# Performance work log

Hardware: AMD Instinct MI355X
Metric: run time of the kernel (lower is better)

Reference implementation:

```python
import jax, jax.numpy as jnp
import numpy as np

B, C, T = 8, 8, 2048
WIN = 512
F_BINS = WIN // 2 + 1  # 257
H, NH = 256, 4
DH = H // NH
EPS = 1e-4


def _ln(x, g, b):
    m = jnp.mean(x, -1, keepdims=True)
    v = jnp.var(x, -1, keepdims=True)
    return (x - m) / jnp.sqrt(v + 1e-5) * g + b


def setup_inputs() -> dict:
    key = jax.random.key(0)
    ks = jax.random.split(key, 16)
    w = lambda i, shape: jax.random.normal(ks[i], shape, jnp.float32) * 0.02
    return {
        'x': jax.random.normal(ks[0], (B, C, T, F_BINS), jnp.float32),
        'W_in': w(1, (F_BINS, H)), 'b_in': jnp.zeros((H,), jnp.float32),
        'W_out': w(2, (H, F_BINS)), 'b_out': jnp.zeros((F_BINS,), jnp.float32),
        'Wq': w(3, (H, H)), 'bq': jnp.zeros((H,), jnp.float32),
        'Wk': w(4, (H, H)), 'bk': jnp.zeros((H,), jnp.float32),
        'Wv': w(5, (H, H)), 'bv': jnp.zeros((H,), jnp.float32),
        'Wo': w(6, (H, H)), 'bo': jnp.zeros((H,), jnp.float32),
        'ln1_g': jnp.ones((H,), jnp.float32), 'ln1_b': jnp.zeros((H,), jnp.float32),
        'Wf1': w(7, (H, WIN)), 'bf1': jnp.zeros((WIN,), jnp.float32),
        'Wf2': w(8, (WIN, H)), 'bf2': jnp.zeros((H,), jnp.float32),
        'ln2_g': jnp.ones((H,), jnp.float32), 'ln2_b': jnp.zeros((H,), jnp.float32),
        'Ws1': w(9, (H, H // 2)), 'bs1': jnp.zeros((H // 2,), jnp.float32),
        'Ws2': w(10, (H // 2, 1)), 'bs2': jnp.zeros((1,), jnp.float32),
        'ps_a': jnp.zeros((1,), jnp.float32), 'ps_b': jnp.ones((1,), jnp.float32),
    }


def _forward(x, W_in, b_in, W_out, b_out, Wq, bq, Wk, bk, Wv, bv, Wo, bo,
             ln1_g, ln1_b, Wf1, bf1, Wf2, bf2, ln2_g, ln2_b,
             Ws1, bs1, Ws2, bs2, ps_a, ps_b):
    lin1 = jax.nn.relu(x @ W_in + b_in)  # [B,C,T,H]
    b, c, t, h_dim = lin1.shape

    def encoder(q, kv):
        # q: [B,T,H], kv: [B,Cc,T,H]; per-time-frame attention over channels
        cc = kv.shape[1]
        Q = (q @ Wq + bq).reshape(b, t, NH, DH)
        K = (kv @ Wk + bk).reshape(b, cc, t, NH, DH)
        V = (kv @ Wv + bv).reshape(b, cc, t, NH, DH)
        scores = jnp.einsum('bthd,bcthd->bthc', Q, K) / jnp.sqrt(jnp.float32(DH))
        A = jax.nn.softmax(scores, axis=-1)
        ctx = jnp.einsum('bthc,bcthd->bthd', A, V).reshape(b, t, h_dim)
        h1 = _ln(q + ctx @ Wo + bo, ln1_g, ln1_b)
        f = jax.nn.relu(h1 @ Wf1 + bf1) @ Wf2 + bf2
        return _ln(h1 + f, ln2_g, ln2_b)

    def seen_enough(hh):
        s = jax.nn.relu(hh @ Ws1 + bs1) @ Ws2 + bs2
        return jax.nn.sigmoid((s - ps_a) / (ps_b + 1e-8))

    still = jnp.ones((b, t, 1), jnp.float32)
    cum = jnp.zeros((b, t, 1), jnp.float32)
    rem = jnp.ones((b, t, 1), jnp.float32)
    pc = jnp.zeros((b, t, 1), jnp.float32)
    out = jnp.zeros((b, t, h_dim), jnp.float32)
    gate = jnp.float32(1.0)  # replicates data-dependent early break

    for ci in range(c):  # small fixed loop over mic channels (ACT ponder)
        hh = encoder(lin1[:, ci], lin1[:, :ci + 1])
        cur = seen_enough(hh) if ci < c - 1 else jnp.ones((b, t, 1), jnp.float32)
        cum_n = cum + cur * still
        pc_n = pc + still
        still_n = (cum_n < 1 - EPS).astype(jnp.float32)
        out_n = out + hh * (cur * still_n + rem * (1 - still_n))
        rem_n = rem - cur * still_n
        pc_n = pc_n + rem_n * (1 - still_n)
        live = gate > 0.5
        cum = jnp.where(live, cum_n, cum)
        pc = jnp.where(live, pc_n, pc)
        out = jnp.where(live, out_n, out)
        rem = jnp.where(live, rem_n, rem)
        still = jnp.where(live, still_n, still)
        gate = gate * (jnp.sum(still) >= EPS).astype(jnp.float32)

    encoder_out = jax.nn.relu(out @ W_out + b_out)  # [B,T,F]
    return encoder_out, pc[:, :, 0]


def reference(x, W_in, b_in, W_out, b_out, Wq, bq, Wk, bk, Wv, bv, Wo, bo,
              ln1_g, ln1_b, Wf1, bf1, Wf2, bf2, ln2_g, ln2_b,
              Ws1, bs1, Ws2, bs2, ps_a, ps_b):
    return _forward(x, W_in, b_in, W_out, b_out, Wq, bq, Wk, bk, Wv, bv, Wo, bo,
                    ln1_g, ln1_b, Wf1, bf1, Wf2, bf2, ln2_g, ln2_b,
                    Ws1, bs1, Ws2, bs2, ps_a, ps_b)
```

## Files before the change

kernel.cpp:

```cpp
#include <hip/hip_runtime.h>
#include <hip/hip_bf16.h>
#include <math.h>

typedef _Float16 f16;
typedef _Float16 f16x4 __attribute__((ext_vector_type(4)));
typedef _Float16 f16x8 __attribute__((ext_vector_type(8)));
typedef float f32x16 __attribute__((ext_vector_type(16)));

constexpr int CH = 8;
constexpr int TT = 2048;
constexpr int FB = 257;
constexpr int HD = 256;
constexpr int DHD = 64;
constexpr int WN = 512;
constexpr int HF = 128;
constexpr int RR = 8 * TT;
constexpr int KXP = 288;

template<int ACT, int WF32, int WF16, int QKV, int XSRC>
__global__ __launch_bounds__(256, 2) void gemm2(
    const f16* __restrict__ Ahi, const f16* __restrict__ Alo, int K,
    const float* __restrict__ Axf, long agrp,
    const f16* __restrict__ Bp,
    const float* __restrict__ bias, const float* __restrict__ bias1,
    const float* __restrict__ bias2,
    float* __restrict__ C0, float* __restrict__ C1, float* __restrict__ C2,
    int ldc, f16* __restrict__ Chi, f16* __restrict__ Clo, int ldf,
    int Nreal, const int* __restrict__ alive)
{
  if (alive && *alive == 0) return;
  __shared__ f16 As[2][2][128][40];
  const int tid = threadIdx.x;
  const int m0 = blockIdx.x * 128;
  const int n0 = blockIdx.y * 64;
  const int q = tid & 3, r = tid >> 2;
  const int lane = tid & 63, wm = tid >> 6;
  const int lr = lane & 31, lg = lane >> 5;
  const int nb0 = n0 >> 5, kd8 = K >> 3;

  f32x16 acc[2];
  #pragma unroll
  for (int nf = 0; nf < 2; nf++)
    #pragma unroll
    for (int g = 0; g < 16; g++) acc[nf][g] = 0.f;

  const long aoff = (long)(m0 + r) * K + q * 8;
  const long hstep = (long)64 * K;
  const float* xR0 = nullptr;
  const float* xR1 = nullptr;
  if constexpr (XSRC) {
    const int r0 = m0 + r, r1 = r0 + 64;
    xR0 = Axf + (long)(r0 >> 11) * agrp + (long)(r0 & 2047) * FB;
    xR1 = Axf + (long)(r1 >> 11) * agrp + (long)(r1 & 2047) * FB;
  }

  f16x8 sA[4];
  auto loadA = [&](int k0) {
    if constexpr (XSRC) {
      float a0[8], a1[8];
      #pragma unroll
      for (int j = 0; j < 8; j++) {
        const int k = k0 + q * 8 + j;
        a0[j] = (k < FB) ? xR0[k] : 0.f;
        a1[j] = (k < FB) ? xR1[k] : 0.f;
      }
      #pragma unroll
      for (int j = 0; j < 8; j++) {
        const f16 h0 = (f16)a0[j]; sA[0][j] = h0; sA[2][j] = (f16)(a0[j] - (float)h0);
        const f16 h1 = (f16)a1[j]; sA[1][j] = h1; sA[3][j] = (f16)(a1[j] - (float)h1);
      }
    } else {
      const long a = aoff + k0;
      sA[0] = *(const f16x8*)(Ahi + a);  sA[1] = *(const f16x8*)(Ahi + a + hstep);
      sA[2] = *(const f16x8*)(Alo + a);  sA[3] = *(const f16x8*)(Alo + a + hstep);
    }
  };
  auto loadB = [&](f16x8 B[2][2][2], int k0) {
    const int kb = (k0 >> 3) + lg;
    #pragma unroll
    for (int kh = 0; kh < 2; kh++)
      #pragma unroll
      for (int nf = 0; nf < 2; nf++)
        #pragma unroll
        for (int hl = 0; hl < 2; hl++)
          B[kh][nf][hl] = *(const f16x8*)(Bp +
              ((long)((nb0 + nf) * kd8 + kb + kh * 2) * 512 + hl * 256 + lr * 8));
  };
  auto kstep = [&](f16x8 SB[2][2][2], f16x8 TB[2][2][2], int k0, int d) {
    *(f16x8*)&As[d][0][r][q * 8]      = sA[0];
    *(f16x8*)&As[d][0][r + 64][q * 8] = sA[1];
    *(f16x8*)&As[d][1][r][q * 8]      = sA[2];
    *(f16x8*)&As[d][1][r + 64][q * 8] = sA[3];
    __syncthreads();
    if (k0 + 32 < K) { loadA(k0 + 32); loadB(TB, k0 + 32); }
    f16x8 fa[2][2];
    #pragma unroll
    for (int kh = 0; kh < 2; kh++)
      #pragma unroll
      for (int hl = 0; hl < 2; hl++)
        fa[kh][hl] = *(const f16x8*)&As[d][hl][wm * 32 + lr][kh * 16 + lg * 8];
    #pragma unroll
    for (int kh = 0; kh < 2; kh++)
      #pragma unroll
      for (int nf = 0; nf < 2; nf++) {
        acc[nf] = __builtin_amdgcn_mfma_f32_32x32x16_f16(fa[kh][1], SB[kh][nf][0], acc[nf], 0, 0, 0);
        acc[nf] = __builtin_amdgcn_mfma_f32_32x32x16_f16(fa[kh][0], SB[kh][nf][1], acc[nf], 0, 0, 0);
        acc[nf] = __builtin_amdgcn_mfma_f32_32x32x16_f16(fa[kh][0], SB[kh][nf][0], acc[nf], 0, 0, 0);
      }
  };

  f16x8 B0[2][2][2], B1[2][2][2];
  loadA(0);
  loadB(B0, 0);
  int d = 0;
  for (int k0 = 0; k0 < K; k0 += 64) {
    kstep(B0, B1, k0, d); d ^= 1;
    if (k0 + 32 < K) { kstep(B1, B0, k0 + 32, d); d ^= 1; }
  }

  #pragma unroll
  for (int nf = 0; nf < 2; nf++) {
    const int col = n0 + nf * 32 + lr;
    const float* bp = bias;
    float* Cp = C0;
    int cc = col;
    if (QKV) {
      const int sel = col >> 8;
      cc = col & 255;
      Cp = sel == 0 ? C0 : (sel == 1 ? C1 : C2);
      bp = sel == 0 ? bias : (sel == 1 ? bias1 : bias2);
    }
    const float bb = (col < Nreal) ? bp[cc] : 0.f;
    #pragma unroll
    for (int g = 0; g < 16; g++) {
      const long row = m0 + wm * 32 + (g & 3) + 8 * (g >> 2) + 4 * lg;
      float v = acc[nf][g] + bb;
      if (ACT) v = fmaxf(v, 0.f);
      if (col < Nreal) {
        if (WF32) Cp[row * (long)ldc + cc] = v;
        if (WF16) {
          const f16 hi = (f16)v;
          Chi[row * (long)ldf + col] = hi;
          Clo[row * (long)ldf + col] = (f16)(v - (float)hi);
        }
      }
    }
  }
}

__global__ __launch_bounds__(512) void gemm_ln(
    const f16* __restrict__ Ahi, const f16* __restrict__ Alo, int K,
    const f16* __restrict__ Bp, const float* __restrict__ bias,
    const f16* __restrict__ Rhi, const f16* __restrict__ Rlo,
    const float* __restrict__ gg, const float* __restrict__ bb_,
    f16* __restrict__ Ohi, f16* __restrict__ Olo,
    const int* __restrict__ alive)
{
  if (alive && *alive == 0) return;
  __shared__ f16 As[2][2][64][40];
  __shared__ float red[64][4][2];
  const int tid = threadIdx.x;
  const int m0 = blockIdx.x * 64;
  const int lane = tid & 63, wave = tid >> 6;
  const int wm = wave & 1, wn = wave >> 1;
  const int lr = lane & 31, lg = lane >> 5;
  const int srow = tid >> 3, sk = (tid & 7) * 4;
  const int kd8 = K >> 3;

  f32x16 acc[2];
  #pragma unroll
  for (int nf = 0; nf < 2; nf++)
    #pragma unroll
    for (int g = 0; g < 16; g++) acc[nf][g] = 0.f;

  const f16* arh = Ahi + (long)(m0 + srow) * K + sk;
  const f16* arl = Alo + (long)(m0 + srow) * K + sk;
  f16x4 sAh, sAl;
  auto loadA = [&](int k0) {
    sAh = *(const f16x4*)(arh + k0);
    sAl = *(const f16x4*)(arl + k0);
  };
  auto loadB = [&](f16x8 B[2][2][2], int k0) {
    const int kb = (k0 >> 3) + lg;
    #pragma unroll
    for (int kh = 0; kh < 2; kh++)
      #pragma unroll
      for (int nf = 0; nf < 2; nf++)
        #pragma unroll
        for (int hl = 0; hl < 2; hl++)
          B[kh][nf][hl] = *(const f16x8*)(Bp +
              ((long)((wn * 2 + nf) * kd8 + kb + kh * 2) * 512 + hl * 256 + lr * 8));
  };
  auto kstep = [&](f16x8 SB[2][2][2], f16x8 TB[2][2][2], int k0, int d) {
    *(f16x4*)&As[d][0][srow][sk] = sAh;
    *(f16x4*)&As[d][1][srow][sk] = sAl;
    __syncthreads();
    if (k0 + 32 < K) { loadA(k0 + 32); loadB(TB, k0 + 32); }
    f16x8 fa[2][2];
    #pragma unroll
    for (int kh = 0; kh < 2; kh++)
      #pragma unroll
      for (int hl = 0; hl < 2; hl++)
        fa[kh][hl] = *(const f16x8*)&As[d][hl][wm * 32 + lr][kh * 16 + lg * 8];
    #pragma unroll
    for (int kh = 0; kh < 2; kh++)
      #pragma unroll
      for (int nf = 0; nf < 2; nf++) {
        acc[nf] = __builtin_amdgcn_mfma_f32_32x32x16_f16(fa[kh][1], SB[kh][nf][0], acc[nf], 0, 0, 0);
        acc[nf] = __builtin_amdgcn_mfma_f32_32x32x16_f16(fa[kh][0], SB[kh][nf][1], acc[nf], 0, 0, 0);
        acc[nf] = __builtin_amdgcn_mfma_f32_32x32x16_f16(fa[kh][0], SB[kh][nf][0], acc[nf], 0, 0, 0);
      }
  };

  f16x8 B0[2][2][2], B1[2][2][2];
  loadA(0);
  loadB(B0, 0);
  int d = 0;
  for (int k0 = 0; k0 < K; k0 += 64) {
    kstep(B0, B1, k0, d); d ^= 1;
    if (k0 + 32 < K) { kstep(B1, B0, k0 + 32, d); d ^= 1; }
  }

  float pr[16], qr[16];
  #pragma unroll
  for (int g = 0; g < 16; g++) {
    const int row_l = wm * 32 + (g & 3) + 8 * (g >> 2) + 4 * lg;
    const long rbase = (long)(m0 + row_l) * HD;
    float s = 0.f, sq = 0.f;
    #pragma unroll
    for (int nf = 0; nf < 2; nf++) {
      const int col = wn * 64 + nf * 32 + lr;
      float v = acc[nf][g] + bias[col]
              + (float)Rhi[rbase + col] + (float)Rlo[rbase + col];
      acc[nf][g] = v;
      s += v; sq += v * v;
    }
    pr[g] = s; qr[g] = sq;
  }
  #pragma unroll
  for (int g = 0; g < 16; g++)
    #pragma unroll
    for (int i = 1; i <= 16; i <<= 1) {
      pr[g] += __shfl_xor(pr[g], i, 64);
      qr[g] += __shfl_xor(qr[g], i, 64);
    }
  if (lr == 0) {
    #pragma unroll
    for (int g = 0; g < 16; g++) {
      const int row_l = wm * 32 + (g & 3) + 8 * (g >> 2) + 4 * lg;
      red[row_l][wn][0] = pr[g];
      red[row_l][wn][1] = qr[g];
    }
  }
  __syncthreads();
  #pragma unroll
  for (int g = 0; g < 16; g++) {
    const int row_l = wm * 32 + (g & 3) + 8 * (g >> 2) + 4 * lg;
    const float mean = (red[row_l][0][0] + red[row_l][1][0] +
                        red[row_l][2][0] + red[row_l][3][0]) * (1.f / HD);
    const float ex2 = (red[row_l][0][1] + red[row_l][1][1] +
                       red[row_l][2][1] + red[row_l][3][1]) * (1.f / HD);
    const float inv = 1.f / sqrtf(ex2 - mean * mean + 1e-5f);
    const long rbase = (long)(m0 + row_l) * HD;
    #pragma unroll
    for (int nf = 0; nf < 2; nf++) {
      const int col = wn * 64 + nf * 32 + lr;
      const float o = (acc[nf][g] - mean) * inv * gg[col] + bb_[col];
      const f16 hi = (f16)o;
      Ohi[rbase + col] = hi;
      Olo[rbase + col] = (f16)(o - (float)hi);
    }
  }
}

template<int FIRST>
__global__ __launch_bounds__(256) void s1_act(
    const f16* __restrict__ hhhi, const f16* __restrict__ hhlo,
    const f16* __restrict__ Bp, const float* __restrict__ bs1,
    const float* __restrict__ Ws2, const float* __restrict__ bs2,
    const float* __restrict__ psa, const float* __restrict__ psb,
    float* __restrict__ cum, float* __restrict__ rem,
    float* __restrict__ still, float* __restrict__ pc,
    f16* __restrict__ outhi, f16* __restrict__ outlo,
    float* __restrict__ pcdst,
    const int* __restrict__ alive, int* __restrict__ myFlag)
{
  if (!FIRST && alive && *alive == 0) return;
  __shared__ f16 As[2][2][64][40];
  __shared__ float red[64][2];
  const int tid = threadIdx.x;
  const int m0 = blockIdx.x * 64;
  const int lane = tid & 63, wave = tid >> 6;
  const int wm = wave & 1, wn = wave >> 1;
  const int lr = lane & 31, lg = lane >> 5;
  const int srow = tid >> 2, sk = (tid & 3) * 8;
  const int K = HD, kd8 = K >> 3;

  f32x16 acc[2];
  #pragma unroll
  for (int nf = 0; nf < 2; nf++)
    #pragma unroll
    for (int g = 0; g < 16; g++) acc[nf][g] = 0.f;

  const f16* arh = hhhi + (long)(m0 + srow) * K + sk;
  const f16* arl = hhlo + (long)(m0 + srow) * K + sk;
  f16x8 sAh, sAl;
  auto loadA = [&](int k0) {
    sAh = *(const f16x8*)(arh + k0);
    sAl = *(const f16x8*)(arl + k0);
  };
  auto loadB = [&](f16x8 B[2][2][2], int k0) {
    const int kb = (k0 >> 3) + lg;
    #pragma unroll
    for (int kh = 0; kh < 2; kh++)
      #pragma unroll
      for (int nf = 0; nf < 2; nf++)
        #pragma unroll
        for (int hl = 0; hl < 2; hl++)
          B[kh][nf][hl] = *(const f16x8*)(Bp +
              ((long)((wn * 2 + nf) * kd8 + kb + kh * 2) * 512 + hl * 256 + lr * 8));
  };
  auto kstep = [&](f16x8 SB[2][2][2], f16x8 TB[2][2][2], int k0, int d) {
    *(f16x8*)&As[d][0][srow][sk] = sAh;
    *(f16x8*)&As[d][1][srow][sk] = sAl;
    __syncthreads();
    if (k0 + 32 < K) { loadA(k0 + 32); loadB(TB, k0 + 32); }
    f16x8 fa[2][2];
    #pragma unroll
    for (int kh = 0; kh < 2; kh++)
      #pragma unroll
      for (int hl = 0; hl < 2; hl++)
        fa[kh][hl] = *(const f16x8*)&As[d][hl][wm * 32 + lr][kh * 16 + lg * 8];
    #pragma unroll
    for (int kh = 0; kh < 2; kh++)
      #pragma unroll
      for (int nf = 0; nf < 2; nf++) {
        acc[nf] = __builtin_amdgcn_mfma_f32_32x32x16_f16(fa[kh][1], SB[kh][nf][0], acc[nf], 0, 0, 0);
        acc[nf] = __builtin_amdgcn_mfma_f32_32x32x16_f16(fa[kh][0], SB[kh][nf][1], acc[nf], 0, 0, 0);
        acc[nf] = __builtin_amdgcn_mfma_f32_32x32x16_f16(fa[kh][0], SB[kh][nf][0], acc[nf], 0, 0, 0);
      }
  };

  f16x8 B0[2][2][2], B1[2][2][2];
  loadA(0);
  loadB(B0, 0);
  int d = 0;
  for (int k0 = 0; k0 < K; k0 += 64) {
    kstep(B0, B1, k0, d); d ^= 1;
    if (k0 + 32 < K) { kstep(B1, B0, k0 + 32, d); d ^= 1; }
  }

  float pr[16];
  #pragma unroll
  for (int g = 0; g < 16; g++) {
    float s = 0.f;
    #pragma unroll
    for (int nf = 0; nf < 2; nf++) {
      const int col = wn * 64 + nf * 32 + lr;
      const float v = fmaxf(acc[nf][g] + bs1[col], 0.f);
      s += v * Ws2[col];
    }
    pr[g] = s;
  }
  #pragma unroll
  for (int g = 0; g < 16; g++)
    #pragma unroll
    for (int i = 1; i <= 16; i <<= 1) pr[g] += __shfl_xor(pr[g], i, 64);
  if (lr == 0) {
    #pragma unroll
    for (int g = 0; g < 16; g++) {
      const int row_l = wm * 32 + (g & 3) + 8 * (g >> 2) + 4 * lg;
      red[row_l][wn] = pr[g];
    }
  }
  __syncthreads();

  const float ipsb = 1.f / (psb[0] + 1e-8f);
  const float pa = psa[0], b2 = bs2[0];
  for (int row_l = 0; row_l < 64; row_l++) {
    const long rg = m0 + row_l;
    const float s = red[row_l][0] + red[row_l][1] + b2;
    const float curv = 1.f / (1.f + expf(-(s - pa) * ipsb));
    const float cu = FIRST ? 0.f : cum[rg];
    const float re = FIRST ? 1.f : rem[rg];
    const float st = FIRST ? 1.f : still[rg];
    const float pp = FIRST ? 0.f : pc[rg];
    const float cum_n = cu + curv * st;
    float pc_n = pp + st;
    const float still_n = (cum_n < 0.9999f) ? 1.f : 0.f;
    const float wgt = curv * still_n + re * (1.f - still_n);
    const long idx = rg * HD + tid;
    const float prev = FIRST ? 0.f : ((float)outhi[idx] + (float)outlo[idx]);
    const float hhv = (float)hhhi[idx] + (float)hhlo[idx];
    const float newv = prev + hhv * wgt;
    const f16 hi = (f16)newv;
    outhi[idx] = hi;
    outlo[idx] = (f16)(newv - (float)hi);
    const float rem_n = re - curv * still_n;
    pc_n += rem_n * (1.f - still_n);
    if (tid == 0) {
      cum[rg] = cum_n; rem[rg] = rem_n; still[rg] = still_n; pc[rg] = pc_n;
      pcdst[rg] = pc_n;
      if (still_n > 0.5f) *myFlag = 1;
    }
  }
}

__global__ __launch_bounds__(256) void act_last(
    const f16* __restrict__ hhhi, const f16* __restrict__ hhlo,
    float* __restrict__ cum, float* __restrict__ rem,
    float* __restrict__ still, float* __restrict__ pc,
    f16* __restrict__ outhi, f16* __restrict__ outlo,
    float* __restrict__ pcdst, const int* __restrict__ alive)
{
  if (alive && *alive == 0) return;
  const int tid = threadIdx.x;
  for (int rr = 0; rr < 8; rr++) {
    const long r = (long)blockIdx.x * 8 + rr;
    const float re = rem[r], st = still[r];
    const float cum_n = cum[r] + st;
    float pc_n = pc[r] + st;
    const float still_n = (cum_n < 0.9999f) ? 1.f : 0.f;
    const float wgt = still_n + re * (1.f - still_n);
    const long idx = r * HD + tid;
    const float newv = (float)outhi[idx] + (float)outlo[idx]
                     + ((float)hhhi[idx] + (float)hhlo[idx]) * wgt;
    const f16 hi = (f16)newv;
    outhi[idx] = hi;
    outlo[idx] = (f16)(newv - (float)hi);
    const float rem_n = re - still_n;
    pc_n += rem_n * (1.f - still_n);
    if (tid == 0) {
      cum[r] = cum_n; rem[r] = rem_n; still[r] = still_n; pc[r] = pc_n;
      pcdst[r] = pc_n;
    }
  }
}

__global__ __launch_bounds__(256) void wsplit_k(
    const float* __restrict__ W_in, const float* __restrict__ Wq,
    const float* __restrict__ Wk, const float* __restrict__ Wv,
    const float* __restrict__ Wo, const float* __restrict__ Wf1,
    const float* __restrict__ Wf2, const float* __restrict__ Ws1,
    const float* __restrict__ Wout,
    f16* __restrict__ WinP, f16* __restrict__ WqkvP, f16* __restrict__ WoP,
    f16* __restrict__ Wf1P, f16* __restrict__ Wf2P, f16* __restrict__ Ws1P,
    f16* __restrict__ WoutP)
{
  const int y = blockIdx.y;
  const long idx = (long)blockIdx.x * 256 + threadIdx.x;
  int Npad, Kpad, Ksrc;
  f16* dst;
  switch (y) {
    case 0: Npad = 256; Kpad = 288; Ksrc = 257; dst = WinP;  break;
    case 1: Npad = 768; Kpad = 256; Ksrc = 256; dst = WqkvP; break;
    case 2: Npad = 256; Kpad = 256; Ksrc = 256; dst = WoP;   break;
    case 3: Npad = 512; Kpad = 256; Ksrc = 256; dst = Wf1P;  break;
    case 4: Npad = 256; Kpad = 512; Ksrc = 512; dst = Wf2P;  break;
    case 5: Npad = 128; Kpad = 256; Ksrc = 256; dst = Ws1P;  break;
    default: Npad = 384; Kpad = 256; Ksrc = 256; dst = WoutP; break;
  }
  if (idx >= (long)Npad * Kpad) return;
  const int n = (int)(idx / Kpad), k = (int)(idx % Kpad);
  float v = 0.f;
  if (k < Ksrc) {
    switch (y) {
      case 0: v = W_in[(long)k * 256 + n]; break;
      case 1: { const int sel = n >> 8;
                const float* s = sel == 0 ? Wq : (sel == 1 ? Wk : Wv);
                v = s[(long)k * 256 + (n & 255)]; } break;
      case 2: v = Wo[(long)k * 256 + n]; break;
      case 3: v = Wf1[(long)k * 512 + n]; break;
      case 4: v = Wf2[(long)k * 256 + n]; break;
      case 5: v = Ws1[(long)k * 128 + n]; break;
      default: v = (n < 257) ? Wout[(long)k * 257 + n] : 0.f; break;
    }
  }
  const long base = ((long)(n >> 5) * (Kpad >> 3) + (k >> 3)) * 512 + (n & 31) * 8 + (k & 7);
  const f16 hi = (f16)v;
  dst[base] = hi;
  dst[base + 256] = (f16)(v - (float)hi);
}

template<int NCc>
__global__ __launch_bounds__(256) void attn_k(
    const float* __restrict__ Q, const float* __restrict__ Ksp,
    const float* __restrict__ Vsp, f16* __restrict__ chi,
    f16* __restrict__ clo, const int* __restrict__ alive)
{
  if (alive && *alive == 0) return;
  const int w = threadIdx.x >> 6;
  const int l = threadIdx.x & 63;
  for (int rr = 0; rr < 4; rr++) {
    const long r = (long)blockIdx.x * 4 + rr;
    const float qv = Q[r * HD + w * DHD + l];
    float sc[NCc];
    #pragma unroll
    for (int c = 0; c < NCc; c++) {
      float p = qv * Ksp[((long)c * RR + r) * HD + w * DHD + l];
      #pragma unroll
      for (int s = 32; s > 0; s >>= 1) p += __shfl_xor(p, s, 64);
      sc[c] = p * 0.125f;
    }
    float m = sc[0];
    #pragma unroll
    for (int c = 1; c < NCc; c++) m = fmaxf(m, sc[c]);
    float a[NCc];
    float den = 0.f;
    #pragma unroll
    for (int c = 0; c < NCc; c++) { a[c] = expf(sc[c] - m); den += a[c]; }
    float cv = 0.f;
    #pragma unroll
    for (int c = 0; c < NCc; c++)
      cv = fmaf(a[c] / den, Vsp[((long)c * RR + r) * HD + w * DHD + l], cv);
    const f16 hi = (f16)cv;
    chi[r * HD + w * DHD + l] = hi;
    clo[r * HD + w * DHD + l] = (f16)(cv - (float)hi);
  }
}

__global__ void init_k(int* flags) {
  if (threadIdx.x < 8) flags[threadIdx.x] = 0;
}

extern "C" void kernel_launch(void* const* d_in, const int* in_sizes, int n_in,
                              void* d_out, int out_size, void* d_ws, size_t ws_size,
                              hipStream_t stream) {
  const float* x    = (const float*)d_in[0];
  const float* W_in = (const float*)d_in[1];
  const float* b_in = (const float*)d_in[2];
  const float* W_out= (const float*)d_in[3];
  const float* b_out= (const float*)d_in[4];
  const float* Wq   = (const float*)d_in[5];
  const float* bq   = (const float*)d_in[6];
  const float* Wk   = (const float*)d_in[7];
  const float* bk   = (const float*)d_in[8];
  const float* Wv   = (const float*)d_in[9];
  const float* bv   = (const float*)d_in[10];
  const float* Wo   = (const float*)d_in[11];
  const float* bo   = (const float*)d_in[12];
  const float* ln1g = (const float*)d_in[13];
  const float* ln1b = (const float*)d_in[14];
  const float* Wf1  = (const float*)d_in[15];
  const float* bf1  = (const float*)d_in[16];
  const float* Wf2  = (const float*)d_in[17];
  const float* bf2  = (const float*)d_in[18];
  const float* ln2g = (const float*)d_in[19];
  const float* ln2b = (const float*)d_in[20];
  const float* Ws1  = (const float*)d_in[21];
  const float* bs1  = (const float*)d_in[22];
  const float* Ws2  = (const float*)d_in[23];
  const float* bs2  = (const float*)d_in[24];
  const float* psa  = (const float*)d_in[25];
  const float* psb  = (const float*)d_in[26];

  float* ws = (float*)d_ws;
  long off = 0;
  auto alloc = [&](long n) { float* p = ws + off; off += n; return p; };
  float* Ks   = alloc((long)CH * RR * HD);
  float* Vs   = alloc((long)CH * RR * HD);
  float* Qb   = alloc((long)RR * HD);
  f16* lin1hi = (f16*)alloc((long)RR * HD / 2);
  f16* lin1lo = (f16*)alloc((long)RR * HD / 2);
  f16* ctxhi  = (f16*)alloc((long)RR * HD / 2);
  f16* ctxlo  = (f16*)alloc((long)RR * HD / 2);
  f16* h1hi   = (f16*)alloc((long)RR * HD / 2);
  f16* h1lo   = (f16*)alloc((long)RR * HD / 2);
  f16* hhhi   = (f16*)alloc((long)RR * HD / 2);
  f16* hhlo   = (f16*)alloc((long)RR * HD / 2);
  f16* t1hi   = (f16*)alloc((long)RR * WN / 2);
  f16* t1lo   = (f16*)alloc((long)RR * WN / 2);
  f16* outhi  = (f16*)alloc((long)RR * HD / 2);
  f16* outlo  = (f16*)alloc((long)RR * HD / 2);
  f16* WinP   = (f16*)alloc(2 * 256 * 288 / 2);
  f16* WqkvP  = (f16*)alloc(2 * 768 * 256 / 2);
  f16* WoP    = (f16*)alloc(2 * 256 * 256 / 2);
  f16* Wf1P   = (f16*)alloc(2 * 512 * 256 / 2);
  f16* Wf2P   = (f16*)alloc(2 * 256 * 512 / 2);
  f16* Ws1P   = (f16*)alloc(2 * 128 * 256 / 2);
  f16* WoutP  = (f16*)alloc(2 * 384 * 256 / 2);
  float* cum  = alloc(RR);
  float* rem  = alloc(RR);
  float* still= alloc(RR);
  float* pc   = alloc(RR);
  int* flags  = (int*)alloc(8);

  init_k<<<1, 256, 0, stream>>>(flags);
  wsplit_k<<<dim3(768, 7), 256, 0, stream>>>(
      W_in, Wq, Wk, Wv, Wo, Wf1, Wf2, Ws1, W_out,
      WinP, WqkvP, WoP, Wf1P, Wf2P, Ws1P, WoutP);

  float* pcdst = (float*)d_out + (long)RR * FB;

  for (int ci = 0; ci < CH; ci++) {
    const int* al = (ci == 0) ? nullptr : (flags + ci - 1);
    gemm2<1, 0, 1, 0, 1><<<dim3(128, 4), 256, 0, stream>>>(
        nullptr, nullptr, KXP, x + (long)ci * TT * FB, (long)CH * TT * FB,
        WinP, b_in, b_in, b_in, nullptr, nullptr, nullptr, HD,
        lin1hi, lin1lo, HD, HD, al);
    gemm2<0, 1, 0, 1, 0><<<dim3(128, 12), 256, 0, stream>>>(
        lin1hi, lin1lo, HD, nullptr, 0, WqkvP, bq, bk, bv,
        Qb, Ks + (long)ci * RR * HD, Vs + (long)ci * RR * HD, HD,
        nullptr, nullptr, HD, 768, al);
    switch (ci) {
      case 0: attn_k<1><<<4096, 256, 0, stream>>>(Qb, Ks, Vs, ctxhi, ctxlo, al); break;
      case 1: attn_k<2><<<4096, 256, 0, stream>>>(Qb, Ks, Vs, ctxhi, ctxlo, al); break;
      case 2: attn_k<3><<<4096, 256, 0, stream>>>(Qb, Ks, Vs, ctxhi, ctxlo, al); break;
      case 3: attn_k<4><<<4096, 256, 0, stream>>>(Qb, Ks, Vs, ctxhi, ctxlo, al); break;
      case 4: attn_k<5><<<4096, 256, 0, stream>>>(Qb, Ks, Vs, ctxhi, ctxlo, al); break;
      case 5: attn_k<6><<<4096, 256, 0, stream>>>(Qb, Ks, Vs, ctxhi, ctxlo, al); break;
      case 6: attn_k<7><<<4096, 256, 0, stream>>>(Qb, Ks, Vs, ctxhi, ctxlo, al); break;
      default: attn_k<8><<<4096, 256, 0, stream>>>(Qb, Ks, Vs, ctxhi, ctxlo, al); break;
    }
    gemm_ln<<<256, 512, 0, stream>>>(
        ctxhi, ctxlo, HD, WoP, bo, lin1hi, lin1lo, ln1g, ln1b,
        h1hi, h1lo, al);
    gemm2<1, 0, 1, 0, 0><<<dim3(128, 8), 256, 0, stream>>>(
        h1hi, h1lo, HD, nullptr, 0, Wf1P, bf1, bf1, bf1,
        nullptr, nullptr, nullptr, WN, t1hi, t1lo, WN, WN, al);
    gemm_ln<<<256, 512, 0, stream>>>(
        t1hi, t1lo, WN, Wf2P, bf2, h1hi, h1lo, ln2g, ln2b,
        hhhi, hhlo, al);
    if (ci == 0)
      s1_act<1><<<256, 256, 0, stream>>>(
          hhhi, hhlo, Ws1P, bs1, Ws2, bs2, psa, psb,
          cum, rem, still, pc, outhi, outlo, pcdst, nullptr, flags + 0);
    else if (ci < CH - 1)
      s1_act<0><<<256, 256, 0, stream>>>(
          hhhi, hhlo, Ws1P, bs1, Ws2, bs2, psa, psb,
          cum, rem, still, pc, outhi, outlo, pcdst, al, flags + ci);
    else
      act_last<<<2048, 256, 0, stream>>>(
          hhhi, hhlo, cum, rem, still, pc, outhi, outlo, pcdst, al);
  }
  gemm2<1, 1, 0, 0, 0><<<dim3(128, 6), 256, 0, stream>>>(
      outhi, outlo, HD, nullptr, 0, WoutP, b_out, b_out, b_out,
      (float*)d_out, nullptr, nullptr, FB, nullptr, nullptr, HD, FB, nullptr);
}
```

Baseline: 853.5 us.

## Fuse input projection with QKV GEMM and FFN pair into single LDS-resident kernels

Adds a lin1_qkv kernel that computes the input linear layer for a 64-row tile, keeps the split-f16 result in shared memory, and immediately runs the Q/K/V projections from it. Adds an ffn_ln kernel that computes the two FFN GEMMs plus residual LayerNorm per 64-row tile, holding the 512-wide intermediate in shared memory in two halves. Together these remove the t1 global buffer, the re-reading of lin1 from global memory, and two kernel launches per channel. In exchange each block uses large shared memory and fewer blocks run (256 blocks of 512 threads), which may lower occupancy and give less parallelism than the separate tiled GEMMs.

```diff
diff --git a/kernel.cpp b/kernel.cpp
--- a/kernel.cpp
+++ b/kernel.cpp
@@ -17,18 +17,17 @@
 constexpr int RR = 8 * TT;
 constexpr int KXP = 288;
 
-template<int ACT, int WF32, int WF16, int QKV, int XSRC>
+#define MFMA3(ACCV, AH, AL, BH, BL)                                            \
+  ACCV = __builtin_amdgcn_mfma_f32_32x32x16_f16(AL, BH, ACCV, 0, 0, 0);        \
+  ACCV = __builtin_amdgcn_mfma_f32_32x32x16_f16(AH, BL, ACCV, 0, 0, 0);        \
+  ACCV = __builtin_amdgcn_mfma_f32_32x32x16_f16(AH, BH, ACCV, 0, 0, 0);
+
+template<int ACT>
 __global__ __launch_bounds__(256, 2) void gemm2(
     const f16* __restrict__ Ahi, const f16* __restrict__ Alo, int K,
-    const float* __restrict__ Axf, long agrp,
-    const f16* __restrict__ Bp,
-    const float* __restrict__ bias, const float* __restrict__ bias1,
-    const float* __restrict__ bias2,
-    float* __restrict__ C0, float* __restrict__ C1, float* __restrict__ C2,
-    int ldc, f16* __restrict__ Chi, f16* __restrict__ Clo, int ldf,
-    int Nreal, const int* __restrict__ alive)
+    const f16* __restrict__ Bp, const float* __restrict__ bias,
+    float* __restrict__ C0, int ldc, int Nreal)
 {
-  if (alive && *alive == 0) return;
   __shared__ f16 As[2][2][128][40];
   const int tid = threadIdx.x;
   const int m0 = blockIdx.x * 128;
@@ -46,34 +45,11 @@
 
   const long aoff = (long)(m0 + r) * K + q * 8;
   const long hstep = (long)64 * K;
-  const float* xR0 = nullptr;
-  const float* xR1 = nullptr;
-  if constexpr (XSRC) {
-    const int r0 = m0 + r, r1 = r0 + 64;
-    xR0 = Axf + (long)(r0 >> 11) * agrp + (long)(r0 & 2047) * FB;
-    xR1 = Axf + (long)(r1 >> 11) * agrp + (long)(r1 & 2047) * FB;
-  }
-
   f16x8 sA[4];
   auto loadA = [&](int k0) {
-    if constexpr (XSRC) {
-      float a0[8], a1[8];
-      #pragma unroll
-      for (int j = 0; j < 8; j++) {
-        const int k = k0 + q * 8 + j;
-        a0[j] = (k < FB) ? xR0[k] : 0.f;
-        a1[j] = (k < FB) ? xR1[k] : 0.f;
-      }
-      #pragma unroll
-      for (int j = 0; j < 8; j++) {
-        const f16 h0 = (f16)a0[j]; sA[0][j] = h0; sA[2][j] = (f16)(a0[j] - (float)h0);
-        const f16 h1 = (f16)a1[j]; sA[1][j] = h1; sA[3][j] = (f16)(a1[j] - (float)h1);
-      }
-    } else {
-      const long a = aoff + k0;
-      sA[0] = *(const f16x8*)(Ahi + a);  sA[1] = *(const f16x8*)(Ahi + a + hstep);
-      sA[2] = *(const f16x8*)(Alo + a);  sA[3] = *(const f16x8*)(Alo + a + hstep);
-    }
+    const long a = aoff + k0;
+    sA[0] = *(const f16x8*)(Ahi + a);  sA[1] = *(const f16x8*)(Ahi + a + hstep);
+    sA[2] = *(const f16x8*)(Alo + a);  sA[3] = *(const f16x8*)(Alo + a + hstep);
   };
   auto loadB = [&](f16x8 B[2][2][2], int k0) {
     const int kb = (k0 >> 3) + lg;
@@ -103,9 +79,7 @@
     for (int kh = 0; kh < 2; kh++)
       #pragma unroll
       for (int nf = 0; nf < 2; nf++) {
-        acc[nf] = __builtin_amdgcn_mfma_f32_32x32x16_f16(fa[kh][1], SB[kh][nf][0], acc[nf], 0, 0, 0);
-        acc[nf] = __builtin_amdgcn_mfma_f32_32x32x16_f16(fa[kh][0], SB[kh][nf][1], acc[nf], 0, 0, 0);
-        acc[nf] = __builtin_amdgcn_mfma_f32_32x32x16_f16(fa[kh][0], SB[kh][nf][0], acc[nf], 0, 0, 0);
+        MFMA3(acc[nf], fa[kh][0], fa[kh][1], SB[kh][nf][0], SB[kh][nf][1]);
       }
   };
 
@@ -121,29 +95,344 @@
   #pragma unroll
   for (int nf = 0; nf < 2; nf++) {
     const int col = n0 + nf * 32 + lr;
-    const float* bp = bias;
-    float* Cp = C0;
-    int cc = col;
-    if (QKV) {
-      const int sel = col >> 8;
-      cc = col & 255;
-      Cp = sel == 0 ? C0 : (sel == 1 ? C1 : C2);
-      bp = sel == 0 ? bias : (sel == 1 ? bias1 : bias2);
-    }
-    const float bb = (col < Nreal) ? bp[cc] : 0.f;
+    const float bb = (col < Nreal) ? bias[col] : 0.f;
     #pragma unroll
     for (int g = 0; g < 16; g++) {
       const long row = m0 + wm * 32 + (g & 3) + 8 * (g >> 2) + 4 * lg;
       float v = acc[nf][g] + bb;
       if (ACT) v = fmaxf(v, 0.f);
-      if (col < Nreal) {
-        if (WF32) Cp[row * (long)ldc + cc] = v;
-        if (WF16) {
-          const f16 hi = (f16)v;
-          Chi[row * (long)ldf + col] = hi;
-          Clo[row * (long)ldf + col] = (f16)(v - (float)hi);
+      if (col < Nreal) C0[row * (long)ldc + col] = v;
+    }
+  }
+}
+
+__global__ __launch_bounds__(512) void lin1_qkv(
+    const float* __restrict__ x, long agrp,
+    const f16* __restrict__ WinP, const float* __restrict__ b_in,
+    const f16* __restrict__ WqkvP, const float* __restrict__ bq,
+    const float* __restrict__ bk, const float* __restrict__ bv,
+    f16* __restrict__ lin1hi, f16* __restrict__ lin1lo,
+    float* __restrict__ Qb, float* __restrict__ Ksd, float* __restrict__ Vsd,
+    const int* __restrict__ alive)
+{
+  if (alive && *alive == 0) return;
+  __shared__ f16 As[2][2][64][40];
+  __shared__ f16 L1[2][64][264];
+  const int tid = threadIdx.x;
+  const int m0 = blockIdx.x * 64;
+  const int lane = tid & 63, wave = tid >> 6;
+  const int wm = wave & 1, wn = wave >> 1;
+  const int lr = lane & 31, lg = lane >> 5;
+  const int srow = tid >> 3, sk = (tid & 7) * 4;
+
+  const int r0 = m0 + srow;
+  const float* xrow = x + (long)(r0 >> 11) * agrp + (long)(r0 & 2047) * FB;
+
+  f16x4 sAh, sAl;
+  auto loadA = [&](int k0) {
+    float v[4];
+    #pragma unroll
+    for (int j = 0; j < 4; j++) {
+      const int k = k0 + sk + j;
+      v[j] = (k < FB) ? xrow[k] : 0.f;
+    }
+    #pragma unroll
+    for (int j = 0; j < 4; j++) {
+      const f16 h = (f16)v[j];
+      sAh[j] = h; sAl[j] = (f16)(v[j] - (float)h);
+    }
+  };
+  auto loadB1 = [&](f16x8 B[2][2][2], int k0) {
+    const int kb = (k0 >> 3) + lg;
+    #pragma unroll
+    for (int kh = 0; kh < 2; kh++)
+      #pragma unroll
+      for (int nf = 0; nf < 2; nf++)
+        #pragma unroll
+        for (int hl = 0; hl < 2; hl++)
+          B[kh][nf][hl] = *(const f16x8*)(WinP +
+              ((long)((wn * 2 + nf) * 36 + kb + kh * 2) * 512 + hl * 256 + lr * 8));
+  };
+
+  f32x16 acc[2];
+  #pragma unroll
+  for (int nf = 0; nf < 2; nf++)
+    #pragma unroll
+    for (int g = 0; g < 16; g++) acc[nf][g] = 0.f;
+
+  auto kstep1 = [&](f16x8 SB[2][2][2], f16x8 TB[2][2][2], int k0, int d) {
+    *(f16x4*)&As[d][0][srow][sk] = sAh;
+    *(f16x4*)&As[d][1][srow][sk] = sAl;
+    __syncthreads();
+    if (k0 + 32 < KXP) { loadA(k0 + 32); loadB1(TB, k0 + 32); }
+    f16x8 fa[2][2];
+    #pragma unroll
+    for (int kh = 0; kh < 2; kh++)
+      #pragma unroll
+      for (int hl = 0; hl < 2; hl++)
+        fa[kh][hl] = *(const f16x8*)&As[d][hl][wm * 32 + lr][kh * 16 + lg * 8];
+    #pragma unroll
+    for (int kh = 0; kh < 2; kh++)
+      #pragma unroll
+      for (int nf = 0; nf < 2; nf++) {
+        MFMA3(acc[nf], fa[kh][0], fa[kh][1], SB[kh][nf][0], SB[kh][nf][1]);
+      }
+  };
+
+  f16x8 B0[2][2][2], B1[2][2][2];
+  loadA(0);
+  loadB1(B0, 0);
+  #pragma unroll
+  for (int s = 0; s < 9; s++) {
+    if ((s & 1) == 0) kstep1(B0, B1, s * 32, 0);
+    else              kstep1(B1, B0, s * 32, 1);
+  }
+
+  #pragma unroll
+  for (int nf = 0; nf < 2; nf++) {
+    const int col = wn * 64 + nf * 32 + lr;
+    const float bb = b_in[col];
+    #pragma unroll
+    for (int g = 0; g < 16; g++) {
+      const int row_l = wm * 32 + (g & 3) + 8 * (g >> 2) + 4 * lg;
+      const float v = fmaxf(acc[nf][g] + bb, 0.f);
+      const f16 hi = (f16)v;
+      const f16 lo = (f16)(v - (float)hi);
+      L1[0][row_l][col] = hi;
+      L1[1][row_l][col] = lo;
+      const long gi = (long)(m0 + row_l) * HD + col;
+      lin1hi[gi] = hi;
+      lin1lo[gi] = lo;
+    }
+  }
+  __syncthreads();
+
+  auto loadB2 = [&](f16x8 B[2][2][2], int k0, int sel) {
+    const int kb = (k0 >> 3) + lg;
+    #pragma unroll
+    for (int kh = 0; kh < 2; kh++)
+      #pragma unroll
+      for (int nf = 0; nf < 2; nf++)
+        #pragma unroll
+        for (int hl = 0; hl < 2; hl++)
+          B[kh][nf][hl] = *(const f16x8*)(WqkvP +
+              ((long)((sel * 8 + wn * 2 + nf) * 32 + kb + kh * 2) * 512 + hl * 256 + lr * 8));
+  };
+  #pragma unroll
+  for (int sel = 0; sel < 3; sel++) {
+    f32x16 a2[2];
+    #pragma unroll
+    for (int nf = 0; nf < 2; nf++)
+      #pragma unroll
+      for (int g = 0; g < 16; g++) a2[nf][g] = 0.f;
+    f16x8 Bc[2][2][2], Bn[2][2][2];
+    loadB2(Bc, 0, sel);
+    #pragma unroll
+    for (int s = 0; s < 8; s++) {
+      const int k0 = s * 32;
+      if (s < 7) loadB2((s & 1) ? Bc : Bn, k0 + 32, sel);
+      f16x8 fa[2][2];
+      #pragma unroll
+      for (int kh = 0; kh < 2; kh++)
+        #pragma unroll
+        for (int hl = 0; hl < 2; hl++)
+          fa[kh][hl] = *(const f16x8*)&L1[hl][wm * 32 + lr][k0 + kh * 16 + lg * 8];
+      #pragma unroll
+      for (int kh = 0; kh < 2; kh++)
+        #pragma unroll
+        for (int nf = 0; nf < 2; nf++) {
+          if (s & 1) { MFMA3(a2[nf], fa[kh][0], fa[kh][1], Bn[kh][nf][0], Bn[kh][nf][1]); }
+          else       { MFMA3(a2[nf], fa[kh][0], fa[kh][1], Bc[kh][nf][0], Bc[kh][nf][1]); }
         }
+    }
+    float* dst = sel == 0 ? Qb : (sel == 1 ? Ksd : Vsd);
+    const float* bp = sel == 0 ? bq : (sel == 1 ? bk : bv);
+    #pragma unroll
+    for (int nf = 0; nf < 2; nf++) {
+      const int col = wn * 64 + nf * 32 + lr;
+      const float bb = bp[col];
+      #pragma unroll
+      for (int g = 0; g < 16; g++) {
+        const int row_l = wm * 32 + (g & 3) + 8 * (g >> 2) + 4 * lg;
+        dst[(long)(m0 + row_l) * HD + col] = a2[nf][g] + bb;
       }
+    }
+  }
+}
+
+__global__ __launch_bounds__(512) void ffn_ln(
+    const f16* __restrict__ h1hi, const f16* __restrict__ h1lo,
+    const f16* __restrict__ Wf1P, const float* __restrict__ bf1,
+    const f16* __restrict__ Wf2P, const float* __restrict__ bf2,
+    const float* __restrict__ g2, const float* __restrict__ b2,
+    f16* __restrict__ hhhi, f16* __restrict__ hhlo,
+    const int* __restrict__ alive)
+{
+  if (alive && *alive == 0) return;
+  __shared__ f16 H1[2][64][264];
+  __shared__ f16 T1[2][64][264];
+  __shared__ float red[64][4][2];
+  const int tid = threadIdx.x;
+  const int m0 = blockIdx.x * 64;
+  const int lane = tid & 63, wave = tid >> 6;
+  const int wm = wave & 1, wn = wave >> 1;
+  const int lr = lane & 31, lg = lane >> 5;
+
+  {
+    const int srow = tid >> 3, scg = (tid & 7) * 32;
+    const long hb = (long)(m0 + srow) * HD + scg;
+    #pragma unroll
+    for (int j = 0; j < 4; j++) {
+      *(f16x8*)&H1[0][srow][scg + j * 8] = *(const f16x8*)(h1hi + hb + j * 8);
+      *(f16x8*)&H1[1][srow][scg + j * 8] = *(const f16x8*)(h1lo + hb + j * 8);
+    }
+  }
+  __syncthreads();
+
+  auto loadBf1 = [&](f16x8 B[2][2][2], int k0, int p) {
+    const int kb = (k0 >> 3) + lg;
+    #pragma unroll
+    for (int kh = 0; kh < 2; kh++)
+      #pragma unroll
+      for (int nf = 0; nf < 2; nf++)
+        #pragma unroll
+        for (int hl = 0; hl < 2; hl++)
+          B[kh][nf][hl] = *(const f16x8*)(Wf1P +
+              ((long)((p * 8 + wn * 2 + nf) * 32 + kb + kh * 2) * 512 + hl * 256 + lr * 8));
+  };
+  auto loadBf2 = [&](f16x8 B[2][2][2], int k0, int p) {
+    const int kb = p * 32 + (k0 >> 3) + lg;
+    #pragma unroll
+    for (int kh = 0; kh < 2; kh++)
+      #pragma unroll
+      for (int nf = 0; nf < 2; nf++)
+        #pragma unroll
+        for (int hl = 0; hl < 2; hl++)
+          B[kh][nf][hl] = *(const f16x8*)(Wf2P +
+              ((long)((wn * 2 + nf) * 64 + kb + kh * 2) * 512 + hl * 256 + lr * 8));
+  };
+
+  f32x16 hacc[2];
+  #pragma unroll
+  for (int nf = 0; nf < 2; nf++)
+    #pragma unroll
+    for (int g = 0; g < 16; g++) hacc[nf][g] = 0.f;
+
+  #pragma unroll
+  for (int p = 0; p < 2; p++) {
+    f32x16 ta[2];
+    #pragma unroll
+    for (int nf = 0; nf < 2; nf++)
+      #pragma unroll
+      for (int g = 0; g < 16; g++) ta[nf][g] = 0.f;
+    {
+      f16x8 Bc[2][2][2], Bn[2][2][2];
+      loadBf1(Bc, 0, p);
+      #pragma unroll
+      for (int s = 0; s < 8; s++) {
+        const int k0 = s * 32;
+        if (s < 7) loadBf1((s & 1) ? Bc : Bn, k0 + 32, p);
+        f16x8 fa[2][2];
+        #pragma unroll
+        for (int kh = 0; kh < 2; kh++)
+          #pragma unroll
+          for (int hl = 0; hl < 2; hl++)
+            fa[kh][hl] = *(const f16x8*)&H1[hl][wm * 32 + lr][k0 + kh * 16 + lg * 8];
+        #pragma unroll
+        for (int kh = 0; kh < 2; kh++)
+          #pragma unroll
+          for (int nf = 0; nf < 2; nf++) {
+            if (s & 1) { MFMA3(ta[nf], fa[kh][0], fa[kh][1], Bn[kh][nf][0], Bn[kh][nf][1]); }
+            else       { MFMA3(ta[nf], fa[kh][0], fa[kh][1], Bc[kh][nf][0], Bc[kh][nf][1]); }
+          }
+      }
+    }
+    __syncthreads();
+    #pragma unroll
+    for (int nf = 0; nf < 2; nf++) {
+      const int col = wn * 64 + nf * 32 + lr;
+      const float bb = bf1[p * 256 + col];
+      #pragma unroll
+      for (int g = 0; g < 16; g++) {
+        const int row_l = wm * 32 + (g & 3) + 8 * (g >> 2) + 4 * lg;
+        const float v = fmaxf(ta[nf][g] + bb, 0.f);
+        const f16 hi = (f16)v;
+        T1[0][row_l][col] = hi;
+        T1[1][row_l][col] = (f16)(v - (float)hi);
+      }
+    }
+    __syncthreads();
+    {
+      f16x8 Bc[2][2][2], Bn[2][2][2];
+      loadBf2(Bc, 0, p);
+      #pragma unroll
+      for (int s = 0; s < 8; s++) {
+        const int k0 = s * 32;
+        if (s < 7) loadBf2((s & 1) ? Bc : Bn, k0 + 32, p);
+        f16x8 ft[2][2];
+        #pragma unroll
+        for (int kh = 0; kh < 2; kh++)
+          #pragma unroll
+          for (int hl = 0; hl < 2; hl++)
+            ft[kh][hl] = *(const f16x8*)&T1[hl][wm * 32 + lr][k0 + kh * 16 + lg * 8];
+        #pragma unroll
+        for (int kh = 0; kh < 2; kh++)
+          #pragma unroll
+          for (int nf = 0; nf < 2; nf++) {
+            if (s & 1) { MFMA3(hacc[nf], ft[kh][0], ft[kh][1], Bn[kh][nf][0], Bn[kh][nf][1]); }
+            else       { MFMA3(hacc[nf], ft[kh][0], ft[kh][1], Bc[kh][nf][0], Bc[kh][nf][1]); }
+          }
+      }
+    }
+  }
+
+  float pr[16], qr[16];
+  #pragma unroll
+  for (int g = 0; g < 16; g++) {
+    const int row_l = wm * 32 + (g & 3) + 8 * (g >> 2) + 4 * lg;
+    float s = 0.f, sq = 0.f;
+    #pragma unroll
+    for (int nf = 0; nf < 2; nf++) {
+      const int col = wn * 64 + nf * 32 + lr;
+      float v = hacc[nf][g] + bf2[col]
+              + (float)H1[0][row_l][col] + (float)H1[1][row_l][col];
+      hacc[nf][g] = v;
+      s += v; sq += v * v;
+    }
+    pr[g] = s; qr[g] = sq;
+  }
+  #pragma unroll
+  for (int g = 0; g < 16; g++)
+    #pragma unroll
+    for (int i = 1; i <= 16; i <<= 1) {
+      pr[g] += __shfl_xor(pr[g], i, 64);
+      qr[g] += __shfl_xor(qr[g], i, 64);
+    }
+  if (lr == 0) {
+    #pragma unroll
+    for (int g = 0; g < 16; g++) {
+      const int row_l = wm * 32 + (g & 3) + 8 * (g >> 2) + 4 * lg;
+      red[row_l][wn][0] = pr[g];
+      red[row_l][wn][1] = qr[g];
+    }
+  }
+  __syncthreads();
+  #pragma unroll
+  for (int g = 0; g < 16; g++) {
+    const int row_l = wm * 32 + (g & 3) + 8 * (g >> 2) + 4 * lg;
+    const float mean = (red[row_l][0][0] + red[row_l][1][0] +
+                        red[row_l][2][0] + red[row_l][3][0]) * (1.f / HD);
+    const float ex2 = (red[row_l][0][1] + red[row_l][1][1] +
+                       red[row_l][2][1] + red[row_l][3][1]) * (1.f / HD);
+    const float inv = 1.f / sqrtf(ex2 - mean * mean + 1e-5f);
+    const long rbase = (long)(m0 + row_l) * HD;
+    #pragma unroll
+    for (int nf = 0; nf < 2; nf++) {
+      const int col = wn * 64 + nf * 32 + lr;
+      const float o = (hacc[nf][g] - mean) * inv * g2[col] + b2[col];
+      const f16 hi = (f16)o;
+      hhhi[rbase + col] = hi;
+      hhlo[rbase + col] = (f16)(o - (float)hi);
     }
   }
 }
@@ -206,9 +495,7 @@
     for (int kh = 0; kh < 2; kh++)
       #pragma unroll
       for (int nf = 0; nf < 2; nf++) {
-        acc[nf] = __builtin_amdgcn_mfma_f32_32x32x16_f16(fa[kh][1], SB[kh][nf][0], acc[nf], 0, 0, 0);
-        acc[nf] = __builtin_amdgcn_mfma_f32_32x32x16_f16(fa[kh][0], SB[kh][nf][1], acc[nf], 0, 0, 0);
-        acc[nf] = __builtin_amdgcn_mfma_f32_32x32x16_f16(fa[kh][0], SB[kh][nf][0], acc[nf], 0, 0, 0);
+        MFMA3(acc[nf], fa[kh][0], fa[kh][1], SB[kh][nf][0], SB[kh][nf][1]);
       }
   };
 
@@ -335,9 +622,7 @@
     for (int kh = 0; kh < 2; kh++)
       #pragma unroll
       for (int nf = 0; nf < 2; nf++) {
-        acc[nf] = __builtin_amdgcn_mfma_f32_32x32x16_f16(fa[kh][1], SB[kh][nf][0], acc[nf], 0, 0, 0);
-        acc[nf] = __builtin_amdgcn_mfma_f32_32x32x16_f16(fa[kh][0], SB[kh][nf][1], acc[nf], 0, 0, 0);
-        acc[nf] = __builtin_amdgcn_mfma_f32_32x32x16_f16(fa[kh][0], SB[kh][nf][0], acc[nf], 0, 0, 0);
+        MFMA3(acc[nf], fa[kh][0], fa[kh][1], SB[kh][nf][0], SB[kh][nf][1]);
       }
   };
 
@@ -376,10 +661,10 @@
   __syncthreads();
 
   const float ipsb = 1.f / (psb[0] + 1e-8f);
-  const float pa = psa[0], b2 = bs2[0];
+  const float pa = psa[0], b2v = bs2[0];
   for (int row_l = 0; row_l < 64; row_l++) {
     const long rg = m0 + row_l;
-    const float s = red[row_l][0] + red[row_l][1] + b2;
+    const float s = red[row_l][0] + red[row_l][1] + b2v;
     const float curv = 1.f / (1.f + expf(-(s - pa) * ipsb));
     const float cu = FIRST ? 0.f : cum[rg];
     const float re = FIRST ? 1.f : rem[rg];
@@ -568,8 +853,6 @@
   f16* h1lo   = (f16*)alloc((long)RR * HD / 2);
   f16* hhhi   = (f16*)alloc((long)RR * HD / 2);
   f16* hhlo   = (f16*)alloc((long)RR * HD / 2);
-  f16* t1hi   = (f16*)alloc((long)RR * WN / 2);
-  f16* t1lo   = (f16*)alloc((long)RR * WN / 2);
   f16* outhi  = (f16*)alloc((long)RR * HD / 2);
   f16* outlo  = (f16*)alloc((long)RR * HD / 2);
   f16* WinP   = (f16*)alloc(2 * 256 * 288 / 2);
@@ -594,14 +877,11 @@
 
   for (int ci = 0; ci < CH; ci++) {
     const int* al = (ci == 0) ? nullptr : (flags + ci - 1);
-    gemm2<1, 0, 1, 0, 1><<<dim3(128, 4), 256, 0, stream>>>(
-        nullptr, nullptr, KXP, x + (long)ci * TT * FB, (long)CH * TT * FB,
-        WinP, b_in, b_in, b_in, nullptr, nullptr, nullptr, HD,
-        lin1hi, lin1lo, HD, HD, al);
-    gemm2<0, 1, 0, 1, 0><<<dim3(128, 12), 256, 0, stream>>>(
-        lin1hi, lin1lo, HD, nullptr, 0, WqkvP, bq, bk, bv,
-        Qb, Ks + (long)ci * RR * HD, Vs + (long)ci * RR * HD, HD,
-        nullptr, nullptr, HD, 768, al);
+    lin1_qkv<<<256, 512, 0, stream>>>(
+        x + (long)ci * TT * FB, (long)CH * TT * FB,
+        WinP, b_in, WqkvP, bq, bk, bv,
+        lin1hi, lin1lo, Qb,
+        Ks + (long)ci * RR * HD, Vs + (long)ci * RR * HD, al);
     switch (ci) {
       case 0: attn_k<1><<<4096, 256, 0, stream>>>(Qb, Ks, Vs, ctxhi, ctxlo, al); break;
       case 1: attn_k<2><<<4096, 256, 0, stream>>>(Qb, Ks, Vs, ctxhi, ctxlo, al); break;
@@ -615,12 +895,8 @@
     gemm_ln<<<256, 512, 0, stream>>>(
         ctxhi, ctxlo, HD, WoP, bo, lin1hi, lin1lo, ln1g, ln1b,
         h1hi, h1lo, al);
-    gemm2<1, 0, 1, 0, 0><<<dim3(128, 8), 256, 0, stream>>>(
-        h1hi, h1lo, HD, nullptr, 0, Wf1P, bf1, bf1, bf1,
-        nullptr, nullptr, nullptr, WN, t1hi, t1lo, WN, WN, al);
-    gemm_ln<<<256, 512, 0, stream>>>(
-        t1hi, t1lo, WN, Wf2P, bf2, h1hi, h1lo, ln2g, ln2b,
-        hhhi, hhlo, al);
+    ffn_ln<<<256, 512, 0, stream>>>(
+        h1hi, h1lo, Wf1P, bf1, Wf2P, bf2, ln2g, ln2b, hhhi, hhlo, al);
     if (ci == 0)
       s1_act<1><<<256, 256, 0, stream>>>(
           hhhi, hhlo, Ws1P, bs1, Ws2, bs2, psa, psb,
@@ -633,7 +909,6 @@
       act_last<<<2048, 256, 0, stream>>>(
           hhhi, hhlo, cum, rem, still, pc, outhi, outlo, pcdst, al);
   }
-  gemm2<1, 1, 0, 0, 0><<<dim3(128, 6), 256, 0, stream>>>(
-      outhi, outlo, HD, nullptr, 0, WoutP, b_out, b_out, b_out,
-      (float*)d_out, nullptr, nullptr, FB, nullptr, nullptr, HD, FB, nullptr);
+  gemm2<1><<<dim3(128, 6), 256, 0, stream>>>(
+      outhi, outlo, HD, WoutP, b_out, (float*)d_out, FB, FB);
 }
```

Measured after the change: 749.7 us. 12.2% less time.
